# Optimization experiments

Hardware: AMD Instinct MI355X
Metric: run time of the kernel (lower is better)

## Reference

```python
import jax, jax.numpy as jnp
import numpy as np

ENTRY_SIZE = 8192
TUPLE_SIZE = 16
N_NEURONS = ENTRY_SIZE // TUPLE_SIZE            # 512
ADDR_SPACE = 2 ** TUPLE_SIZE                     # 65536
BATCH = 4096


def setup_inputs() -> dict:
    key = jax.random.key(0)
    k1, k2, k3 = jax.random.split(key, 3)
    # Binary input bits [B, entry_size]
    inp = jax.random.randint(k1, (BATCH, ENTRY_SIZE), 0, 2, dtype=jnp.int32)
    # Permutation mapping bits -> tuples (identity permutation; arange fill)
    tuple_mapping = jnp.arange(ENTRY_SIZE, dtype=jnp.int64)
    # Dense RAM tables emulating the per-neuron dicts:
    #   counts[n, a] = number of training samples that hit address a in neuron n
    #                  (0 means the address was never trained -> not in dict)
    #   sums[n, a]   = accumulated target sum for that address
    counts = jax.random.randint(k2, (N_NEURONS, ADDR_SPACE), 0, 4, dtype=jnp.int32)
    sums = jax.random.normal(k3, (N_NEURONS, ADDR_SPACE), dtype=jnp.float32)
    return {"input": inp, "tuple_mapping": tuple_mapping, "counts": counts, "sums": sums}


def reference(input, tuple_mapping, counts, sums):
    """RegressionWisard.predict with centrality='mean'.

    input:  [B, entry_size] binary bits (int32)
    tuple_mapping: [entry_size] permutation (int)
    counts: [n_neurons, 2^tuple_size] int32 RAM hit counts
    sums:   [n_neurons, 2^tuple_size] float32 RAM target sums
    """
    B = input.shape[0]
    # Map and group bits into tuples: [B, N, T]
    mapped = jnp.take(input, tuple_mapping, axis=1).reshape(B, N_NEURONS, TUPLE_SIZE)
    # Binary address per (sample, neuron); tidx flips so bit 0 is the MSB.
    pow2 = (jnp.int32(1) << jnp.arange(TUPLE_SIZE - 1, -1, -1, dtype=jnp.int32))
    addr = jnp.einsum("bnt,t->bn", mapped, pow2)  # [B, N], values in [0, 2^T)
    neuron_idx = jnp.arange(N_NEURONS, dtype=jnp.int32)[None, :]  # [1, N]
    c = counts[neuron_idx, addr]  # [B, N]
    s = sums[neuron_idx, addr]    # [B, N]
    trained = c > 0               # dict-membership (torch.isin) equivalent
    response = jnp.sum(jnp.where(trained, s, jnp.float32(0)), axis=1)      # [B]
    counters = jnp.sum(jnp.where(trained, c, 0), axis=1).astype(s.dtype)   # [B]
    return jnp.nan_to_num(response / counters)
```

## Files before the change

kernel.cpp:

```cpp
#include <hip/hip_runtime.h>


constexpr int BATCH   = 4096;
constexpr int ENTRY   = 8192;
constexpr int TUP     = 16;
constexpr int NEUR    = ENTRY / TUP;
constexpr int THREADS = 256;

__global__ __launch_bounds__(THREADS) void wisard_kernel(
    const int*   __restrict__ input,
    const int*   __restrict__ mapping,
    const int*   __restrict__ counts,
    const float* __restrict__ sums,
    float*       __restrict__ out)
{
    __shared__ unsigned int packed[ENTRY / 32];
    __shared__ float s_resp[THREADS / 64];
    __shared__ int   s_cnt [THREADS / 64];

    const int b    = blockIdx.x;
    const int tid  = threadIdx.x;
    const int lane = tid & 63;
    const int wv   = tid >> 6;

    const int* row = input + (size_t)b * ENTRY;
    #pragma unroll
    for (int i = wv; i < ENTRY / 64; i += THREADS / 64) {
        const int j = i * 64 + lane;
        const unsigned long long m = __ballot(row[j] & 1);
        if (lane == 0) {
            packed[i * 2]     = (unsigned int)(m);
            packed[i * 2 + 1] = (unsigned int)(m >> 32);
        }
    }
    __syncthreads();

    float resp = 0.0f;
    int   cnt  = 0;
    #pragma unroll
    for (int k = 0; k < NEUR / THREADS; ++k) {
        const int n = tid + k * THREADS;
        const int* map_n = mapping + n * TUP;
        int addr = 0;
        #pragma unroll
        for (int t = 0; t < TUP; ++t) {
            const int j = map_n[t];
            const int bit = (packed[j >> 5] >> (j & 31)) & 1;
            addr = (addr << 1) | bit;
        }
        const int idx = (n << 16) | addr;
        const int c = counts[idx];
        if (c > 0) {
            resp += sums[idx];
            cnt  += c;
        }
    }

    #pragma unroll
    for (int off = 32; off > 0; off >>= 1) {
        resp += __shfl_down(resp, off, 64);
        cnt  += __shfl_down(cnt,  off, 64);
    }
    if (lane == 0) { s_resp[wv] = resp; s_cnt[wv] = cnt; }
    __syncthreads();
    if (tid == 0) {
        float r = s_resp[0] + s_resp[1] + s_resp[2] + s_resp[3];
        int   c = s_cnt[0]  + s_cnt[1]  + s_cnt[2]  + s_cnt[3];
        out[b] = (c > 0) ? (r / (float)c) : 0.0f;
    }
}

extern "C" void kernel_launch(void* const* d_in, const int* in_sizes, int n_in,
                              void* d_out, int out_size, void* d_ws, size_t ws_size,
                              hipStream_t stream) {
    (void)in_sizes; (void)n_in; (void)out_size; (void)d_ws; (void)ws_size;
    const int*   input   = (const int*)d_in[0];
    const int*   mapping = (const int*)d_in[1];
    const int*   counts  = (const int*)d_in[2];
    const float* sums    = (const float*)d_in[3];
    float*       out     = (float*)d_out;

    wisard_kernel<<<BATCH, THREADS, 0, stream>>>(input, mapping, counts, sums, out);
}
```

Before: 368.3 us.

## Split into address, LDS-staged per-neuron table lookup, and atomic-reduce phases

Replaces the per-sample kernel, which gathered randomly from the counts and sums tables, with a multi-phase pipeline. Phase A packs several samples' input bits and writes 16-bit addresses in neuron-major order. Phase B streams each eighth of a neuron's table into LDS, with counts narrowed to bytes, and resolves all samples' lookups locally. It accumulates results with 64-bit fixed-point atomics, and a final kernel divides. This trades random HBM gathers for streaming table reads plus global atomics, but depends on workspace size and assumes counts fit in a byte and sums fit the fixed-point range.

```diff
diff --git a/kernel.cpp b/kernel.cpp
--- a/kernel.cpp
+++ b/kernel.cpp
@@ -1,61 +1,166 @@
 #include <hip/hip_runtime.h>
 
+
+typedef float f32x4 __attribute__((ext_vector_type(4)));
+typedef int   i32x4 __attribute__((ext_vector_type(4)));
 
 constexpr int BATCH   = 4096;
 constexpr int ENTRY   = 8192;
 constexpr int TUP     = 16;
 constexpr int NEUR    = ENTRY / TUP;
-constexpr int THREADS = 256;
+constexpr int SPB_A   = 4;
+constexpr int QSPLIT  = 8;
+constexpr int QSIZE   = 65536 / QSPLIT;
 
-__global__ __launch_bounds__(THREADS) void wisard_kernel(
-    const int*   __restrict__ input,
-    const int*   __restrict__ mapping,
-    const int*   __restrict__ counts,
-    const float* __restrict__ sums,
-    float*       __restrict__ out)
+constexpr size_t ADDR_BYTES = (size_t)NEUR * BATCH * 2;
+constexpr size_t ACC_OFF    = ADDR_BYTES;
+constexpr size_t WS_NEED    = ADDR_BYTES + (size_t)BATCH * 8;
+
+__global__ __launch_bounds__(256) void zero_acc_kernel(unsigned long long* acc) {
+    acc[blockIdx.x * 256 + threadIdx.x] = 0ull;
+}
+
+__global__ __launch_bounds__(256) void phaseA_kernel(
+    const int* __restrict__ input,
+    const int* __restrict__ mapping,
+    unsigned short* __restrict__ addr_out)
 {
-    __shared__ unsigned int packed[ENTRY / 32];
-    __shared__ float s_resp[THREADS / 64];
-    __shared__ int   s_cnt [THREADS / 64];
-
-    const int b    = blockIdx.x;
+    __shared__ unsigned int packed[SPB_A][ENTRY / 32];
     const int tid  = threadIdx.x;
     const int lane = tid & 63;
     const int wv   = tid >> 6;
+    const int b0   = blockIdx.x * SPB_A;
+    constexpr int CH = ENTRY / 64;
 
-    const int* row = input + (size_t)b * ENTRY;
+    for (int i0 = wv * 4; i0 < SPB_A * CH; i0 += 16) {
+        int v[4];
+        #pragma unroll
+        for (int u = 0; u < 4; ++u) {
+            const int i = i0 + u, r = i >> 7, c = i & 127;
+            v[u] = __builtin_nontemporal_load(
+                &input[(size_t)(b0 + r) * ENTRY + c * 64 + lane]);
+        }
+        #pragma unroll
+        for (int u = 0; u < 4; ++u) {
+            const int i = i0 + u, r = i >> 7, c = i & 127;
+            const unsigned long long m = __ballot(v[u] & 1);
+            if (lane == 0) {
+                packed[r][c * 2]     = (unsigned int)(m);
+                packed[r][c * 2 + 1] = (unsigned int)(m >> 32);
+            }
+        }
+    }
+    __syncthreads();
+
     #pragma unroll
-    for (int i = wv; i < ENTRY / 64; i += THREADS / 64) {
-        const int j = i * 64 + lane;
-        const unsigned long long m = __ballot(row[j] & 1);
+    for (int k = 0; k < 2; ++k) {
+        const int n = tid + k * 256;
+        const int* map_n = mapping + n * TUP;
+        int addr[SPB_A] = {0, 0, 0, 0};
+        #pragma unroll
+        for (int t = 0; t < TUP; ++t) {
+            const int j = map_n[t];
+            const unsigned w = j >> 5, sh = j & 31;
+            #pragma unroll
+            for (int s = 0; s < SPB_A; ++s)
+                addr[s] = (addr[s] << 1) | ((packed[s][w] >> sh) & 1);
+        }
+        uint2 pk;
+        pk.x = (unsigned)addr[0] | ((unsigned)addr[1] << 16);
+        pk.y = (unsigned)addr[2] | ((unsigned)addr[3] << 16);
+        *(uint2*)(addr_out + (size_t)n * BATCH + b0) = pk;
+    }
+}
+
+__global__ __launch_bounds__(256) void phaseB_kernel(
+    const int*   __restrict__ counts,
+    const float* __restrict__ sums,
+    const unsigned short* __restrict__ addr,
+    unsigned long long* __restrict__ acc)
+{
+    __shared__ float         s_tab[QSIZE];
+    __shared__ unsigned char c_tab[QSIZE];
+    const int tid = threadIdx.x;
+    const int n   = blockIdx.x >> 3;
+    const int q   = blockIdx.x & (QSPLIT - 1);
+    const size_t base = ((size_t)n << 16) + ((size_t)q * QSIZE);
+
+    const f32x4* s4 = (const f32x4*)(sums + base);
+    const i32x4* c4 = (const i32x4*)(counts + base);
+    f32x4 vs[8]; i32x4 vc[8];
+    #pragma unroll
+    for (int i = 0; i < 8; ++i) vs[i] = __builtin_nontemporal_load(&s4[tid + 256 * i]);
+    #pragma unroll
+    for (int i = 0; i < 8; ++i) vc[i] = __builtin_nontemporal_load(&c4[tid + 256 * i]);
+    #pragma unroll
+    for (int i = 0; i < 8; ++i) {
+        ((f32x4*)s_tab)[tid + 256 * i] = vs[i];
+        *(uchar4*)&c_tab[(tid + 256 * i) * 4] =
+            make_uchar4((unsigned char)vc[i].x, (unsigned char)vc[i].y,
+                        (unsigned char)vc[i].z, (unsigned char)vc[i].w);
+    }
+    __syncthreads();
+
+    const unsigned short* arow = addr + ((size_t)n << 12);
+    #pragma unroll
+    for (int i = tid; i < BATCH; i += 256) {
+        const int a = arow[i];
+        if ((a >> 13) == q) {
+            const int local = a & (QSIZE - 1);
+            const int c = c_tab[local];
+            if (c) {
+                const long long r = (long long)__float2int_rn(s_tab[local] * 16777216.0f);
+                atomicAdd(&acc[i], (unsigned long long)((r << 20) + (long long)c));
+            }
+        }
+    }
+}
+
+__global__ __launch_bounds__(256) void phaseC_kernel(
+    const unsigned long long* __restrict__ acc, float* __restrict__ out)
+{
+    const int i = blockIdx.x * 256 + threadIdx.x;
+    const long long v = (long long)acc[i];
+    const int cnt = (int)(v & 0xFFFFF);
+    const long long rq = v >> 20;
+    out[i] = (cnt > 0)
+        ? (float)(((double)rq * (1.0 / 16777216.0)) / (double)cnt)
+        : 0.0f;
+}
+
+__global__ __launch_bounds__(256) void wisard_direct_kernel(
+    const int* __restrict__ input, const int* __restrict__ mapping,
+    const int* __restrict__ counts, const float* __restrict__ sums,
+    float* __restrict__ out)
+{
+    __shared__ unsigned int packed[ENTRY / 32];
+    __shared__ float s_resp[4];
+    __shared__ int   s_cnt [4];
+    const int tid = threadIdx.x, lane = tid & 63, wv = tid >> 6;
+    const int* row = input + (size_t)blockIdx.x * ENTRY;
+    for (int i = wv; i < ENTRY / 64; i += 4) {
+        const unsigned long long m = __ballot(row[i * 64 + lane] & 1);
         if (lane == 0) {
-            packed[i * 2]     = (unsigned int)(m);
+            packed[i * 2] = (unsigned int)m;
             packed[i * 2 + 1] = (unsigned int)(m >> 32);
         }
     }
     __syncthreads();
-
-    float resp = 0.0f;
-    int   cnt  = 0;
+    float resp = 0.0f; int cnt = 0;
     #pragma unroll
-    for (int k = 0; k < NEUR / THREADS; ++k) {
-        const int n = tid + k * THREADS;
+    for (int k = 0; k < 2; ++k) {
+        const int n = tid + k * 256;
         const int* map_n = mapping + n * TUP;
-        int addr = 0;
+        int a = 0;
         #pragma unroll
         for (int t = 0; t < TUP; ++t) {
             const int j = map_n[t];
-            const int bit = (packed[j >> 5] >> (j & 31)) & 1;
-            addr = (addr << 1) | bit;
+            a = (a << 1) | ((packed[j >> 5] >> (j & 31)) & 1);
         }
-        const int idx = (n << 16) | addr;
+        const int idx = (n << 16) | a;
         const int c = counts[idx];
-        if (c > 0) {
-            resp += sums[idx];
-            cnt  += c;
-        }
+        if (c > 0) { resp += sums[idx]; cnt += c; }
     }
-
     #pragma unroll
     for (int off = 32; off > 0; off >>= 1) {
         resp += __shfl_down(resp, off, 64);
@@ -65,20 +170,29 @@
     __syncthreads();
     if (tid == 0) {
         float r = s_resp[0] + s_resp[1] + s_resp[2] + s_resp[3];
-        int   c = s_cnt[0]  + s_cnt[1]  + s_cnt[2]  + s_cnt[3];
-        out[b] = (c > 0) ? (r / (float)c) : 0.0f;
+        int   c = s_cnt[0] + s_cnt[1] + s_cnt[2] + s_cnt[3];
+        out[blockIdx.x] = (c > 0) ? (r / (float)c) : 0.0f;
     }
 }
 
 extern "C" void kernel_launch(void* const* d_in, const int* in_sizes, int n_in,
                               void* d_out, int out_size, void* d_ws, size_t ws_size,
                               hipStream_t stream) {
-    (void)in_sizes; (void)n_in; (void)out_size; (void)d_ws; (void)ws_size;
+    (void)in_sizes; (void)n_in; (void)out_size;
     const int*   input   = (const int*)d_in[0];
     const int*   mapping = (const int*)d_in[1];
     const int*   counts  = (const int*)d_in[2];
     const float* sums    = (const float*)d_in[3];
     float*       out     = (float*)d_out;
 
-    wisard_kernel<<<BATCH, THREADS, 0, stream>>>(input, mapping, counts, sums, out);
+    if (ws_size >= WS_NEED) {
+        unsigned short*     addr_ws = (unsigned short*)d_ws;
+        unsigned long long* acc     = (unsigned long long*)((char*)d_ws + ACC_OFF);
+        zero_acc_kernel<<<BATCH / 256, 256, 0, stream>>>(acc);
+        phaseA_kernel<<<BATCH / SPB_A, 256, 0, stream>>>(input, mapping, addr_ws);
+        phaseB_kernel<<<NEUR * QSPLIT, 256, 0, stream>>>(counts, sums, addr_ws, acc);
+        phaseC_kernel<<<BATCH / 256, 256, 0, stream>>>(acc, out);
+    } else {
+        wisard_direct_kernel<<<BATCH, 256, 0, stream>>>(input, mapping, counts, sums, out);
+    }
 }
```

After: 378.1 us. 2.7% more time.
